# Kernel optimization log

Measured on AMD Instinct MI355X. Metric: run time of the kernel, lower is better.

Reference implementation:

```python
import jax, jax.numpy as jnp
import numpy as np

FP8_MAX = 448.0          # E4M3 max representable
SAFETY_MARGIN = 1.1
SCALE_CAP = 10000.0


def _fp8_scale(t):
    """Per-tensor dynamic scale (single step: tracked amax == current amax)."""
    amax = jax.lax.stop_gradient(jnp.max(jnp.abs(t)))
    scale = FP8_MAX / (amax * SAFETY_MARGIN)
    scale = jnp.where(amax == 0.0, 1.0, jnp.minimum(scale, SCALE_CAP))
    return scale


def _quantize_e4m3(t, scale):
    """Scale, clamp to E4M3 range, round to fp8, return dequantized-to-fp32 codes."""
    ts = jnp.clip(t * scale, -FP8_MAX, FP8_MAX)
    return ts.astype(jnp.float8_e4m3fn).astype(jnp.float32)


def setup_inputs() -> dict:
    key = jax.random.key(0)
    k1, k2, k3 = jax.random.split(key, 3)
    B, S, D_IN, D_OUT = 4, 2048, 4096, 4096
    x = jax.random.normal(k1, (B, S, D_IN), dtype=jnp.float32)
    weight = jax.random.normal(k2, (D_OUT, D_IN), dtype=jnp.float32) * 0.02
    bias = jax.random.normal(k3, (D_OUT,), dtype=jnp.float32) * 0.02
    return {"x": x, "weight": weight, "bias": bias}


def reference(x, weight, bias):
    orig_shape = x.shape
    x2 = x.reshape(-1, orig_shape[-1])               # [M, d_in]

    x_scale = _fp8_scale(x2)
    w_scale = _fp8_scale(weight)

    x_fp8 = _quantize_e4m3(x2, x_scale)              # fp8 codes held in fp32
    w_fp8 = _quantize_e4m3(weight, w_scale)

    # torch._scaled_mm: out = (x_fp8 @ w_fp8^T) * scale_a * scale_b, scale_* = 1/scale
    out = jnp.einsum('mk,nk->mn', x_fp8, w_fp8) * (1.0 / x_scale) * (1.0 / w_scale)
    out = out.reshape(*orig_shape[:-1], out.shape[-1])
    out = out + bias
    return out
```

## Files before the change

### kernel.cpp

```cpp
#include <hip/hip_runtime.h>
#include <hip/hip_bf16.h>

typedef float f32x16 __attribute__((ext_vector_type(16)));
typedef int   i32x8  __attribute__((ext_vector_type(8)));
typedef int   i32x4  __attribute__((ext_vector_type(4)));

#define FP8_MAX 448.0f


__device__ __forceinline__ void g2l16(const void* g, void* l) {
    __builtin_amdgcn_global_load_lds(
        (const __attribute__((address_space(1))) void*)g,
        (__attribute__((address_space(3))) void*)l,
        16, 0, 0);
}

__device__ __forceinline__ float scale_from(float amax) {
    float s = FP8_MAX / (amax * 1.1f);
    return (amax == 0.0f) ? 1.0f : fminf(s, 10000.0f);
}


__global__ void init_kernel(unsigned* amax) {
    amax[0] = 0u;
    amax[1] = 0u;
}

__global__ void amax_fused_kernel(const float* __restrict__ x, size_t nx,
                                  const float* __restrict__ w, size_t nw,
                                  unsigned* __restrict__ amax, int xblocks) {
    const float* src;
    size_t n;
    unsigned* out;
    int bid, nb;
    if ((int)blockIdx.x < xblocks) {
        src = x; n = nx; out = amax; bid = blockIdx.x; nb = xblocks;
    } else {
        src = w; n = nw; out = amax + 1; bid = blockIdx.x - xblocks; nb = gridDim.x - xblocks;
    }
    float m = 0.0f;
    const size_t ustep = (size_t)blockDim.x * 4;
    const size_t chunkf = ustep * 8;
    size_t base = (size_t)bid * chunkf + (size_t)threadIdx.x * 4;
    const size_t gstride = (size_t)nb * chunkf;
    for (; base < n; base += gstride) {
        float4 v[8];
        #pragma unroll
        for (int u = 0; u < 8; ++u) {
            size_t idx = base + (size_t)u * ustep;
            float4 vv = {0.0f, 0.0f, 0.0f, 0.0f};
            if (idx < n) vv = *(const float4*)(src + idx);
            v[u] = vv;
        }
        #pragma unroll
        for (int u = 0; u < 8; ++u)
            m = fmaxf(m, fmaxf(fmaxf(fabsf(v[u].x), fabsf(v[u].y)),
                               fmaxf(fabsf(v[u].z), fabsf(v[u].w))));
    }
    #pragma unroll
    for (int off = 32; off > 0; off >>= 1)
        m = fmaxf(m, __shfl_xor(m, off));
    __shared__ float sm[4];
    if ((threadIdx.x & 63) == 0) sm[threadIdx.x >> 6] = m;
    __syncthreads();
    if (threadIdx.x == 0) {
        float mm = fmaxf(fmaxf(sm[0], sm[1]), fmaxf(sm[2], sm[3]));
        atomicMax(out, __float_as_uint(mm));
    }
}

__device__ __forceinline__ float qclamp(float v, float s) {
    return fminf(fmaxf(v * s, -FP8_MAX), FP8_MAX);
}

__global__ void quant_fused_kernel(const float* __restrict__ x, size_t nx,
                                   const float* __restrict__ w, size_t nw,
                                   const unsigned* __restrict__ amax,
                                   unsigned char* __restrict__ xq,
                                   unsigned char* __restrict__ wq, int xblocks) {
    const float* src;
    size_t n;
    unsigned char* dst;
    int bid, nb, sel;
    if ((int)blockIdx.x < xblocks) {
        src = x; n = nx; dst = xq; bid = blockIdx.x; nb = xblocks; sel = 0;
    } else {
        src = w; n = nw; dst = wq; bid = blockIdx.x - xblocks; nb = gridDim.x - xblocks; sel = 1;
    }
    const float s = scale_from(__uint_as_float(amax[sel]));
    const size_t ustep = (size_t)blockDim.x * 4;
    const size_t chunkf = ustep * 4;
    size_t base = (size_t)bid * chunkf + (size_t)threadIdx.x * 4;
    const size_t gstride = (size_t)nb * chunkf;
    for (; base < n; base += gstride) {
        float4 v[4];
        bool ok[4];
        #pragma unroll
        for (int u = 0; u < 4; ++u) {
            size_t idx = base + (size_t)u * ustep;
            ok[u] = idx < n;
            float4 vv = {0.0f, 0.0f, 0.0f, 0.0f};
            if (ok[u]) vv = *(const float4*)(src + idx);
            v[u] = vv;
        }
        #pragma unroll
        for (int u = 0; u < 4; ++u) {
            if (ok[u]) {
                int p = __builtin_amdgcn_cvt_pk_fp8_f32(qclamp(v[u].x, s), qclamp(v[u].y, s), 0, false);
                p = __builtin_amdgcn_cvt_pk_fp8_f32(qclamp(v[u].z, s), qclamp(v[u].w, s), p, true);
                *(unsigned*)(dst + base + (size_t)u * ustep) = (unsigned)p;
            }
        }
    }
}

#define BM 256
#define BN 256
#define BKB 64

__global__ __launch_bounds__(512, 2) void gemm_fp8_kernel(
    const unsigned char* __restrict__ Aq,
    const unsigned char* __restrict__ Bq,
    const float* __restrict__ bias,
    const unsigned* __restrict__ amax,
    float* __restrict__ out,
    int M, int N, int K) {
    __shared__ alignas(16) unsigned char sA[4][BM * BKB];
    __shared__ alignas(16) unsigned char sB[4][BN * BKB];

    const int tid = threadIdx.x;
    const int wave = tid >> 6;
    const int lane = tid & 63;
    const int r31 = lane & 31;
    const int half = lane >> 5;

    int nwg = (int)gridDim.x;
    int bid = (int)blockIdx.x;
    if ((nwg & 7) == 0) {
        int cpx = nwg >> 3;
        bid = (bid & 7) * cpx + (bid >> 3);
    }
    const int nbn = N / BN;
    const int brow = (bid / nbn) * BM;
    const int bcol = (bid % nbn) * BN;

    const int R0 = (wave >> 2) * 128;
    const int C0 = (wave & 3) * 64;

    f32x16 acc[4][2] = {};

    const int NT = K / BKB;
    const int j0 = tid * 16;

    auto stageA = [&](int slot, int t) {
        #pragma unroll
        for (int j = 0; j < 2; ++j) {
            int oo = j * 8192 + j0;
            int r = oo >> 6;
            int c = (oo & 63) ^ (((r >> 1) & 3) << 4);
            g2l16(Aq + (size_t)(brow + r) * K + t * BKB + c,
                  &sA[slot][j * 8192 + wave * 1024]);
        }
    };
    auto stageB = [&](int slot, int t) {
        #pragma unroll
        for (int j = 0; j < 2; ++j) {
            int oo = j * 8192 + j0;
            int r = oo >> 6;
            int c = (oo & 63) ^ (((r >> 1) & 3) << 4);
            g2l16(Bq + (size_t)(bcol + r) * K + t * BKB + c,
                  &sB[slot][j * 8192 + wave * 1024]);
        }
    };
    auto rdA = [&](int slot, int row) -> i32x8 {
        const unsigned char* base = &sA[slot][row * BKB];
        int swz = ((row >> 1) & 3) << 4;
        int kb = half * 32;
        union { i32x8 v8; i32x4 v4[2]; } u;
        u.v4[0] = *(const i32x4*)(base + (kb ^ swz));
        u.v4[1] = *(const i32x4*)(base + ((kb + 16) ^ swz));
        return u.v8;
    };
    auto rdB = [&](int slot, int row) -> i32x8 {
        const unsigned char* base = &sB[slot][row * BKB];
        int swz = ((row >> 1) & 3) << 4;
        int kb = half * 32;
        union { i32x8 v8; i32x4 v4[2]; } u;
        u.v4[0] = *(const i32x4*)(base + (kb ^ swz));
        u.v4[1] = *(const i32x4*)(base + ((kb + 16) ^ swz));
        return u.v8;
    };

    #define MM(a, b, c) \
        c = __builtin_amdgcn_mfma_scale_f32_32x32x64_f8f6f4( \
            a, b, c, 0, 0, 0, 0x7f7f7f7f, 0, 0x7f7f7f7f)

    stageA(0, 0); stageB(0, 0);
    stageA(1, 1); stageB(1, 1);
    stageA(2, 2); stageB(2, 2);
    asm volatile("s_waitcnt vmcnt(8)" ::: "memory");
    __builtin_amdgcn_s_barrier();

    for (int t = 0; t < NT; ++t) {
        const int s = t & 3;
        i32x8 a[4], b[2];
        #pragma unroll
        for (int m = 0; m < 4; ++m) a[m] = rdA(s, R0 + m * 32 + r31);
        #pragma unroll
        for (int n = 0; n < 2; ++n) b[n] = rdB(s, C0 + n * 32 + r31);

        int tt = t + 3;
        if (tt >= NT) tt -= NT;
        stageA(tt & 3, tt);
        stageB(tt & 3, tt);

        asm volatile("s_waitcnt vmcnt(8)" ::: "memory");
        __builtin_amdgcn_s_barrier();
        asm volatile("s_waitcnt lgkmcnt(0)" ::: "memory");
        __builtin_amdgcn_sched_barrier(0);

        __builtin_amdgcn_s_setprio(1);
        #pragma unroll
        for (int m = 0; m < 4; ++m)
            #pragma unroll
            for (int n = 0; n < 2; ++n)
                MM(a[m], b[n], acc[m][n]);
        __builtin_amdgcn_s_setprio(0);
        __builtin_amdgcn_s_barrier();
    }

    const float invx = 1.0f / scale_from(__uint_as_float(amax[0]));
    const float invw = 1.0f / scale_from(__uint_as_float(amax[1]));
    const float s2 = invx * invw;
    #pragma unroll
    for (int n = 0; n < 2; ++n) {
        int col = bcol + C0 + n * 32 + r31;
        float bv = bias[col];
        #pragma unroll
        for (int m = 0; m < 4; ++m) {
            int rbase = brow + R0 + m * 32 + half * 4;
            #pragma unroll
            for (int r = 0; r < 16; ++r) {
                int row = rbase + (r & 3) + 8 * (r >> 2);
                out[(size_t)row * N + col] = acc[m][n][r] * s2 + bv;
            }
        }
    }
    #undef MM
}


extern "C" void kernel_launch(void* const* d_in, const int* in_sizes, int n_in,
                              void* d_out, int out_size, void* d_ws, size_t ws_size,
                              hipStream_t stream) {
    const float* x    = (const float*)d_in[0];
    const float* w    = (const float*)d_in[1];
    const float* bias = (const float*)d_in[2];
    float* out = (float*)d_out;

    const size_t nx = (size_t)in_sizes[0];
    const size_t nw = (size_t)in_sizes[1];
    const int N = in_sizes[2];
    const int K = (int)(nw / (size_t)N);
    const int M = (int)(nx / (size_t)K);

    unsigned* amax = (unsigned*)d_ws;
    unsigned char* xq = (unsigned char*)d_ws + 256;
    unsigned char* wq = xq + nx;

    const int TOTB = 2048;
    int xb = (int)((double)TOTB * (double)nx / (double)(nx + nw));
    if (xb < 1) xb = 1;
    if (xb > TOTB - 1) xb = TOTB - 1;

    init_kernel<<<1, 1, 0, stream>>>(amax);
    amax_fused_kernel<<<TOTB, 256, 0, stream>>>(x, nx, w, nw, amax, xb);
    quant_fused_kernel<<<TOTB, 256, 0, stream>>>(x, nx, w, nw, amax, xq, wq, xb);

    dim3 grid((M / BM) * (N / BN));
    gemm_fp8_kernel<<<grid, 512, 0, stream>>>(xq, wq, bias, amax, out, M, N, K);
}
```

Before: 236.0 us.

## Double-buffer LDS-to-register fragments and overlap reads with MFMA

Restructures the main K loop to use two register fragment sets: while MFMAs run on the current set, the next tile's fragments are read from LDS. One barrier per iteration is dropped and the loop is unrolled by four so that LDS slot indices become compile-time constants. This is meant to hide LDS read latency behind matrix work, at the cost of higher VGPR pressure and the assumption that NT is a multiple of 4.

Result: no change. 231.7 us (-1.8%).

```diff
diff --git a/kernel.cpp b/kernel.cpp
--- a/kernel.cpp
+++ b/kernel.cpp
@@ -195,39 +195,50 @@
         c = __builtin_amdgcn_mfma_scale_f32_32x32x64_f8f6f4( \
             a, b, c, 0, 0, 0, 0x7f7f7f7f, 0, 0x7f7f7f7f)
 
+    i32x8 aA[4], bA[2], aB[4], bB[2];
+
     stageA(0, 0); stageB(0, 0);
     stageA(1, 1); stageB(1, 1);
     stageA(2, 2); stageB(2, 2);
     asm volatile("s_waitcnt vmcnt(8)" ::: "memory");
     __builtin_amdgcn_s_barrier();
-
-    for (int t = 0; t < NT; ++t) {
-        const int s = t & 3;
-        i32x8 a[4], b[2];
-        #pragma unroll
-        for (int m = 0; m < 4; ++m) a[m] = rdA(s, R0 + m * 32 + r31);
-        #pragma unroll
-        for (int n = 0; n < 2; ++n) b[n] = rdB(s, C0 + n * 32 + r31);
-
-        int tt = t + 3;
-        if (tt >= NT) tt -= NT;
-        stageA(tt & 3, tt);
-        stageB(tt & 3, tt);
-
-        asm volatile("s_waitcnt vmcnt(8)" ::: "memory");
-        __builtin_amdgcn_s_barrier();
-        asm volatile("s_waitcnt lgkmcnt(0)" ::: "memory");
-        __builtin_amdgcn_sched_barrier(0);
-
-        __builtin_amdgcn_s_setprio(1);
-        #pragma unroll
-        for (int m = 0; m < 4; ++m)
-            #pragma unroll
-            for (int n = 0; n < 2; ++n)
-                MM(a[m], b[n], acc[m][n]);
-        __builtin_amdgcn_s_setprio(0);
-        __builtin_amdgcn_s_barrier();
-    }
+    __builtin_amdgcn_sched_barrier(0);
+    #pragma unroll
+    for (int m = 0; m < 4; ++m) aA[m] = rdA(0, R0 + m * 32 + r31);
+    #pragma unroll
+    for (int n = 0; n < 2; ++n) bA[n] = rdB(0, C0 + n * 32 + r31);
+
+    #define HALF(j, CURa, CURb, NXTa, NXTb)                                       \
+    {                                                                             \
+        int t = tb + (j);                                                         \
+        int ts = t + 3;                                                           \
+        if (ts >= NT) ts -= NT;                \
+        stageA(((j) + 3) & 3, ts);                                                \
+        stageB(((j) + 3) & 3, ts);                                                \
+        asm volatile("s_waitcnt vmcnt(8) lgkmcnt(0)" ::: "memory");               \
+        __builtin_amdgcn_s_barrier();                                             \
+        __builtin_amdgcn_sched_barrier(0);                                        \
+        _Pragma("unroll")                                                         \
+        for (int m = 0; m < 4; ++m) NXTa[m] = rdA(((j) + 1) & 3, R0 + m * 32 + r31); \
+        _Pragma("unroll")                                                         \
+        for (int n = 0; n < 2; ++n) NXTb[n] = rdB(((j) + 1) & 3, C0 + n * 32 + r31); \
+        __builtin_amdgcn_sched_barrier(0);    \
+        __builtin_amdgcn_s_setprio(1);                                            \
+        _Pragma("unroll")                                                         \
+        for (int m = 0; m < 4; ++m)                                               \
+            _Pragma("unroll")                                                     \
+            for (int n = 0; n < 2; ++n)                                           \
+                MM(CURa[m], CURb[n], acc[m][n]);                                  \
+        __builtin_amdgcn_s_setprio(0);                                            \
+    }
+
+    for (int tb = 0; tb < NT; tb += 4) {
+        HALF(0, aA, bA, aB, bB)
+        HALF(1, aB, bB, aA, bA)
+        HALF(2, aA, bA, aB, bB)
+        HALF(3, aB, bB, aA, bA)
+    }
+    #undef HALF
 
     const float invx = 1.0f / scale_from(__uint_as_float(amax[0]));
     const float invw = 1.0f / scale_from(__uint_as_float(amax[1]));
```
